# Kernel optimization log

Measured on AMD Instinct MI355X. Metric: run time of the kernel, lower is better.

Reference implementation:

```python
import jax, jax.numpy as jnp
import numpy as np

N_NODES = 100000
IN_DIM = 128
UNITS = 128
BATCH = 16384
N_NEIGH = 25


def setup_inputs() -> dict:
    key = jax.random.key(0)
    ks = jax.random.split(key, 6)
    features = jax.random.normal(ks[0], (N_NODES, IN_DIM), dtype=jnp.float32)
    node = jax.random.randint(ks[1], (BATCH, 1), 0, N_NODES)
    neighbours = jax.random.randint(ks[2], (BATCH, N_NEIGH), 0, N_NODES)
    # learned params
    def glorot(k, shape):
        lim = np.sqrt(6.0 / (shape[0] + shape[1]))
        return jax.random.uniform(k, shape, jnp.float32, -lim, lim)
    node_weights = glorot(ks[3], (IN_DIM, UNITS))
    lstm_W = glorot(ks[4], (IN_DIM, 4 * UNITS))   # kernel: gates [i, f, g, o]
    lstm_U = glorot(ks[5], (UNITS, 4 * UNITS))    # recurrent kernel
    lstm_b = jnp.ones((4 * UNITS,), jnp.float32)  # bias_initializer='ones'
    return {"features": features, "node": node, "neighbours": neighbours,
            "node_weights": node_weights, "lstm_W": lstm_W,
            "lstm_U": lstm_U, "lstm_b": lstm_b}


def _lstm_last_hidden(x_btd, W, U, b, units):
    # x_btd: [B, T, D] -> last hidden state [B, units]; Keras gate order i,f,g,o
    B = x_btd.shape[0]
    # precompute input projections for all steps: [T, B, 4U]
    zx = jnp.einsum('btd,dk->tbk', x_btd, W) + b

    def step(carry, zx_t):
        h, c = carry
        z = zx_t + h @ U
        i, f, g, o = jnp.split(z, 4, axis=-1)
        i = jax.nn.sigmoid(i)
        f = jax.nn.sigmoid(f)
        g = jnp.tanh(g)
        o = jax.nn.sigmoid(o)
        c = f * c + i * g
        h = o * jnp.tanh(c)
        return (h, c), None

    h0 = jnp.zeros((B, units), x_btd.dtype)
    c0 = jnp.zeros((B, units), x_btd.dtype)
    (h, _), _ = jax.lax.scan(step, (h0, c0), zx)
    return h


def reference(features, node, neighbours, node_weights, lstm_W, lstm_U, lstm_b):
    node_feat = features[node[:, 0]]          # [B, D]
    neigh_feat = features[neighbours]         # [B, T, D]
    from_neighs = _lstm_last_hidden(neigh_feat, lstm_W, lstm_U, lstm_b, UNITS)
    from_self = node_feat @ node_weights      # [B, units]
    output = (from_self + from_neighs) / 2
    return jax.nn.relu(output)
```

## Files before the change

kernel.cpp:

```cpp
#include <hip/hip_runtime.h>
#include <hip/hip_bf16.h>


typedef __bf16 bf16;
typedef __bf16 bf16x8 __attribute__((ext_vector_type(8)));
typedef float f32x4 __attribute__((ext_vector_type(4)));

#define FEATS_OFF 262144

__device__ __forceinline__ float fast_sig(float x) {
  float e = __builtin_amdgcn_exp2f(-1.442695041f * x);
  return __builtin_amdgcn_rcpf(1.0f + e);
}
__device__ __forceinline__ float fast_tanh(float x) {
  float e = __builtin_amdgcn_exp2f(-2.885390082f * x);
  return (1.0f - e) * __builtin_amdgcn_rcpf(1.0f + e);
}
__device__ __forceinline__ f32x4 splat4(float x) {
  f32x4 v; v[0] = x; v[1] = x; v[2] = x; v[3] = x; return v;
}
__device__ __forceinline__ bf16x8 pack8(float4 a, float4 b) {
  bf16x8 v;
  v[0] = (bf16)a.x; v[1] = (bf16)a.y; v[2] = (bf16)a.z; v[3] = (bf16)a.w;
  v[4] = (bf16)b.x; v[5] = (bf16)b.y; v[6] = (bf16)b.z; v[7] = (bf16)b.w;
  return v;
}

__global__ void prep_kernel(const float* __restrict__ W, const float* __restrict__ U,
                            const float* __restrict__ NW, bf16* __restrict__ ws) {
  int idx = blockIdx.x * 256 + threadIdx.x;
  if (idx < 131072) {
    const float* __restrict__ src = (idx < 65536) ? W : U;
    int r = idx & 65535;
    int f = r >> 9, lane = (r >> 3) & 63, j = r & 7;
    int kt = f & 3, g = (f >> 2) & 3, w = f >> 4;
    int k = kt * 32 + (lane >> 4) * 8 + j;
    int col = g * 128 + w * 16 + (lane & 15);
    ws[idx] = (bf16)src[k * 512 + col];
  } else {
    int r = idx - 131072;
    int f = r >> 9, lane = (r >> 3) & 63, j = r & 7;
    int kt = f & 3, w = f >> 2;
    int k = kt * 32 + (lane >> 4) * 8 + j;
    int col = w * 16 + (lane & 15);
    ws[idx] = (bf16)NW[k * 128 + col];
  }
}

__global__ void prep_feats(const float4* __restrict__ in, bf16x8* __restrict__ out) {
  int i = blockIdx.x * 256 + threadIdx.x;
  int stride = gridDim.x * 256;
  for (; i < 1600000; i += stride) {
    float4 a = in[2 * i], b = in[2 * i + 1];
    __builtin_nontemporal_store(pack8(a, b), out + i);
  }
}

__global__ __launch_bounds__(512, 2)
void lstm_kernel(const int* __restrict__ node, const int* __restrict__ neigh,
                 const float* __restrict__ bias, const bf16* __restrict__ wsf,
                 float* __restrict__ out) {
  __shared__ char ub[131072];
  __shared__ char xb[16384];
  __shared__ char hb[16384];

  const int tid  = threadIdx.x;
  const int lane = tid & 63;
  const int ug   = tid >> 6;
  const int l15  = lane & 15;
  const int lhi  = lane >> 4;
  const int b0   = blockIdx.x * 64;
  const bf16* __restrict__ fb = wsf + FEATS_OFF;

#pragma unroll
  for (int i = 0; i < 16; ++i) {
    int k = i * 512 + tid;
    ((bf16x8*)ub)[k] = *(const bf16x8*)(wsf + 65536 + k * 8);
  }

  float bb[4];
#pragma unroll
  for (int g = 0; g < 4; ++g) bb[g] = bias[g * 128 + ug * 16 + l15];

  f32x4 cc[4];
#pragma unroll
  for (int m = 0; m < 4; ++m) cc[m] = splat4(0.0f);

  const int gr = tid >> 3;
  const int gq = tid & 7;
  const int xsw = (gr & 7) << 4;
  const int xbase = gr * 256 + gq * 32;
  const int rbase = (b0 + gr) * 25;

  {
    int ni = neigh[rbase];
    const bf16* gsrc = fb + (size_t)ni * 128 + gq * 16;
    *(bf16x8*)(xb + (xbase ^ xsw))        = __builtin_nontemporal_load((const bf16x8*)gsrc);
    *(bf16x8*)(xb + ((xbase + 16) ^ xsw)) = __builtin_nontemporal_load((const bf16x8*)(gsrc + 8));
  }
  int ni_next = neigh[rbase + 1];
  __syncthreads();

  f32x4 acc[4][4];
  const int asw = (l15 & 7) << 4;

  auto mfma_phase = [&](const bf16x8 (&wf)[4][4], bool withH) {
#pragma unroll
    for (int kt = 0; kt < 4; ++kt) {
      bf16x8 ufr[4];
#pragma unroll
      for (int g = 0; g < 4; ++g)
        ufr[g] = *(const bf16x8*)(ub + (((ug * 16 + g * 4 + kt) << 6 | lane) << 4));
      bf16x8 xa[4];
#pragma unroll
      for (int m = 0; m < 4; ++m)
        xa[m] = *(const bf16x8*)(xb + (((m * 16 + l15) * 256 + (kt * 4 + lhi) * 16) ^ asw));
#pragma unroll
      for (int g = 0; g < 4; ++g)
#pragma unroll
        for (int m = 0; m < 4; ++m)
          acc[g][m] = __builtin_amdgcn_mfma_f32_16x16x32_bf16(xa[m], wf[g][kt], acc[g][m], 0, 0, 0);
      if (withH) {
        bf16x8 ha[4];
#pragma unroll
        for (int m = 0; m < 4; ++m)
          ha[m] = *(const bf16x8*)(hb + (((m * 16 + l15) * 256 + (kt * 4 + lhi) * 16) ^ asw));
#pragma unroll
        for (int g = 0; g < 4; ++g)
#pragma unroll
          for (int m = 0; m < 4; ++m)
            acc[g][m] = __builtin_amdgcn_mfma_f32_16x16x32_bf16(ha[m], ufr[g], acc[g][m], 0, 0, 0);
      }
    }
  };

#pragma unroll 1
  for (int t = 0; t < 24; ++t) {
    int ni = ni_next;
    ni_next = (t < 23) ? neigh[rbase + t + 2] : node[b0 + gr];

    bf16x8 wf[4][4];
#pragma unroll
    for (int g = 0; g < 4; ++g)
#pragma unroll
      for (int kt = 0; kt < 4; ++kt)
        wf[g][kt] = *(const bf16x8*)(wsf + (((ug * 4 + g) * 4 + kt) << 9) + (lane << 3));
    __builtin_amdgcn_sched_barrier(0);

    const bf16* gsrc = fb + (size_t)ni * 128 + gq * 16;
    bf16x8 pa = __builtin_nontemporal_load((const bf16x8*)gsrc);
    bf16x8 pb = __builtin_nontemporal_load((const bf16x8*)(gsrc + 8));

#pragma unroll
    for (int g = 0; g < 4; ++g) {
      f32x4 bi = splat4(bb[g]);
#pragma unroll
      for (int m = 0; m < 4; ++m) acc[g][m] = bi;
    }

    if (t == 0) mfma_phase(wf, false); else mfma_phase(wf, true);

    __syncthreads();

    *(bf16x8*)(xb + (xbase ^ xsw))        = pa;
    *(bf16x8*)(xb + ((xbase + 16) ^ xsw)) = pb;

#pragma unroll
    for (int m = 0; m < 4; ++m)
#pragma unroll
      for (int r = 0; r < 4; ++r) {
        float iv = fast_sig(acc[0][m][r]);
        float fv = fast_sig(acc[1][m][r]);
        float gv = fast_tanh(acc[2][m][r]);
        float ov = fast_sig(acc[3][m][r]);
        float cv = fv * cc[m][r] + iv * gv;
        cc[m][r] = cv;
        float hv = ov * fast_tanh(cv);
        int row = m * 16 + lhi * 4 + r;
        *(bf16*)(hb + ((row * 256 + (ug * 16 + l15) * 2) ^ ((row & 7) << 4))) = (bf16)hv;
      }
    __syncthreads();
  }

  float hl[4][4];
  {
    bf16x8 wf[4][4];
#pragma unroll
    for (int g = 0; g < 4; ++g)
#pragma unroll
      for (int kt = 0; kt < 4; ++kt)
        wf[g][kt] = *(const bf16x8*)(wsf + (((ug * 4 + g) * 4 + kt) << 9) + (lane << 3));
    __builtin_amdgcn_sched_barrier(0);

    const bf16* gsrc = fb + (size_t)ni_next * 128 + gq * 16;
    bf16x8 pa = __builtin_nontemporal_load((const bf16x8*)gsrc);
    bf16x8 pb = __builtin_nontemporal_load((const bf16x8*)(gsrc + 8));

#pragma unroll
    for (int g = 0; g < 4; ++g) {
      f32x4 bi = splat4(bb[g]);
#pragma unroll
      for (int m = 0; m < 4; ++m) acc[g][m] = bi;
    }
    mfma_phase(wf, true);

    __syncthreads();

    *(bf16x8*)(xb + (xbase ^ xsw))        = pa;
    *(bf16x8*)(xb + ((xbase + 16) ^ xsw)) = pb;

#pragma unroll
    for (int m = 0; m < 4; ++m)
#pragma unroll
      for (int r = 0; r < 4; ++r) {
        float iv = fast_sig(acc[0][m][r]);
        float fv = fast_sig(acc[1][m][r]);
        float gv = fast_tanh(acc[2][m][r]);
        float ov = fast_sig(acc[3][m][r]);
        float cv = fv * cc[m][r] + iv * gv;
        hl[m][r] = ov * fast_tanh(cv);
      }
    __syncthreads();
  }

  {
    f32x4 accs[4];
#pragma unroll
    for (int m = 0; m < 4; ++m) accs[m] = splat4(0.0f);
#pragma unroll
    for (int kt = 0; kt < 4; ++kt) {
      bf16x8 nwf = *(const bf16x8*)(wsf + 131072 + ((ug * 4 + kt) << 9) + (lane << 3));
      bf16x8 xa[4];
#pragma unroll
      for (int m = 0; m < 4; ++m)
        xa[m] = *(const bf16x8*)(xb + (((m * 16 + l15) * 256 + (kt * 4 + lhi) * 16) ^ asw));
#pragma unroll
      for (int m = 0; m < 4; ++m)
        accs[m] = __builtin_amdgcn_mfma_f32_16x16x32_bf16(xa[m], nwf, accs[m], 0, 0, 0);
    }
#pragma unroll
    for (int m = 0; m < 4; ++m)
#pragma unroll
      for (int r = 0; r < 4; ++r) {
        int row = m * 16 + lhi * 4 + r;
        float v = (accs[m][r] + hl[m][r]) * 0.5f;
        __builtin_nontemporal_store(v > 0.0f ? v : 0.0f,
                                    out + (b0 + row) * 128 + ug * 16 + l15);
      }
  }
}

extern "C" void kernel_launch(void* const* d_in, const int* in_sizes, int n_in,
                              void* d_out, int out_size, void* d_ws, size_t ws_size,
                              hipStream_t stream) {
  const float* feats = (const float*)d_in[0];
  const int*   node  = (const int*)d_in[1];
  const int*   neigh = (const int*)d_in[2];
  const float* nw    = (const float*)d_in[3];
  const float* W     = (const float*)d_in[4];
  const float* U     = (const float*)d_in[5];
  const float* b     = (const float*)d_in[6];
  bf16* ws = (bf16*)d_ws;
  float* out = (float*)d_out;

  prep_kernel<<<576, 256, 0, stream>>>(W, U, nw, ws);
  prep_feats<<<2048, 256, 0, stream>>>((const float4*)feats, (bf16x8*)(ws + FEATS_OFF));
  lstm_kernel<<<256, 512, 0, stream>>>(node, neigh, b, ws, out);
}
```

Measured before the change: 262.6 us.

## Gather neighbour features directly into registers and double-buffer hidden state

Each wave now loads its neighbour feature fragments straight from global memory into MFMA operand registers instead of staging them through shared memory. The hidden-state buffer is double-buffered so each timestep needs only one barrier. The two preprocessing kernels are merged into a single launch. The cost is that every wave redundantly fetches the whole x tile, raising cache traffic, and gather latency now sits inside each step.

```diff
diff --git a/kernel.cpp b/kernel.cpp
--- a/kernel.cpp
+++ b/kernel.cpp
@@ -26,33 +26,34 @@
   return v;
 }
 
-__global__ void prep_kernel(const float* __restrict__ W, const float* __restrict__ U,
-                            const float* __restrict__ NW, bf16* __restrict__ ws) {
-  int idx = blockIdx.x * 256 + threadIdx.x;
-  if (idx < 131072) {
-    const float* __restrict__ src = (idx < 65536) ? W : U;
-    int r = idx & 65535;
-    int f = r >> 9, lane = (r >> 3) & 63, j = r & 7;
-    int kt = f & 3, g = (f >> 2) & 3, w = f >> 4;
-    int k = kt * 32 + (lane >> 4) * 8 + j;
-    int col = g * 128 + w * 16 + (lane & 15);
-    ws[idx] = (bf16)src[k * 512 + col];
-  } else {
-    int r = idx - 131072;
-    int f = r >> 9, lane = (r >> 3) & 63, j = r & 7;
-    int kt = f & 3, w = f >> 2;
-    int k = kt * 32 + (lane >> 4) * 8 + j;
-    int col = w * 16 + (lane & 15);
-    ws[idx] = (bf16)NW[k * 128 + col];
-  }
-}
-
-__global__ void prep_feats(const float4* __restrict__ in, bf16x8* __restrict__ out) {
-  int i = blockIdx.x * 256 + threadIdx.x;
+__global__ void prep_all(const float* __restrict__ W, const float* __restrict__ U,
+                         const float* __restrict__ NW, const float4* __restrict__ feats,
+                         bf16* __restrict__ ws) {
+  int gid = blockIdx.x * 256 + threadIdx.x;
+  if (gid < 147456) {
+    int idx = gid;
+    if (idx < 131072) {
+      const float* __restrict__ src = (idx < 65536) ? W : U;
+      int r = idx & 65535;
+      int f = r >> 9, lane = (r >> 3) & 63, j = r & 7;
+      int kt = f & 3, g = (f >> 2) & 3, w = f >> 4;
+      int k = kt * 32 + (lane >> 4) * 8 + j;
+      int col = g * 128 + w * 16 + (lane & 15);
+      ws[idx] = (bf16)src[k * 512 + col];
+    } else {
+      int r = idx - 131072;
+      int f = r >> 9, lane = (r >> 3) & 63, j = r & 7;
+      int kt = f & 3, w = f >> 2;
+      int k = kt * 32 + (lane >> 4) * 8 + j;
+      int col = w * 16 + (lane & 15);
+      ws[idx] = (bf16)NW[k * 128 + col];
+    }
+  }
+  bf16x8* __restrict__ fo = (bf16x8*)(ws + FEATS_OFF);
   int stride = gridDim.x * 256;
-  for (; i < 1600000; i += stride) {
-    float4 a = in[2 * i], b = in[2 * i + 1];
-    __builtin_nontemporal_store(pack8(a, b), out + i);
+  for (int i = gid; i < 1600000; i += stride) {
+    float4 a = feats[2 * i], b = feats[2 * i + 1];
+    __builtin_nontemporal_store(pack8(a, b), fo + i);
   }
 }
 
@@ -61,8 +62,7 @@
                  const float* __restrict__ bias, const bf16* __restrict__ wsf,
                  float* __restrict__ out) {
   __shared__ char ub[131072];
-  __shared__ char xb[16384];
-  __shared__ char hb[16384];
+  __shared__ char hb[32768];
 
   const int tid  = threadIdx.x;
   const int lane = tid & 63;
@@ -86,45 +86,66 @@
 #pragma unroll
   for (int m = 0; m < 4; ++m) cc[m] = splat4(0.0f);
 
-  const int gr = tid >> 3;
-  const int gq = tid & 7;
-  const int xsw = (gr & 7) << 4;
-  const int xbase = gr * 256 + gq * 32;
-  const int rbase = (b0 + gr) * 25;
-
-  {
-    int ni = neigh[rbase];
-    const bf16* gsrc = fb + (size_t)ni * 128 + gq * 16;
-    *(bf16x8*)(xb + (xbase ^ xsw))        = __builtin_nontemporal_load((const bf16x8*)gsrc);
-    *(bf16x8*)(xb + ((xbase + 16) ^ xsw)) = __builtin_nontemporal_load((const bf16x8*)(gsrc + 8));
-  }
-  int ni_next = neigh[rbase + 1];
+  int niv[4];
+#pragma unroll
+  for (int m = 0; m < 4; ++m) niv[m] = neigh[(b0 + m * 16 + l15) * 25];
+
   __syncthreads();
 
   f32x4 acc[4][4];
   const int asw = (l15 & 7) << 4;
 
-  auto mfma_phase = [&](const bf16x8 (&wf)[4][4], bool withH) {
-#pragma unroll
-    for (int kt = 0; kt < 4; ++kt) {
-      bf16x8 ufr[4];
-#pragma unroll
-      for (int g = 0; g < 4; ++g)
-        ufr[g] = *(const bf16x8*)(ub + (((ug * 16 + g * 4 + kt) << 6 | lane) << 4));
-      bf16x8 xa[4];
-#pragma unroll
-      for (int m = 0; m < 4; ++m)
-        xa[m] = *(const bf16x8*)(xb + (((m * 16 + l15) * 256 + (kt * 4 + lhi) * 16) ^ asw));
-#pragma unroll
-      for (int g = 0; g < 4; ++g)
+  float hl[4][4];
+
+#pragma unroll 1
+  for (int t = 0; t < 25; ++t) {
+    const int pcur = t & 1;
+    const char* hrd = hb + pcur * 16384;
+    char*       hwr = hb + (pcur ^ 1) * 16384;
+
+    bf16x8 xa[4][4];
+#pragma unroll
+    for (int m = 0; m < 4; ++m) {
+      const bf16* bp = fb + (size_t)niv[m] * 128 + lhi * 8;
+#pragma unroll
+      for (int kt = 0; kt < 4; ++kt)
+        xa[m][kt] = __builtin_nontemporal_load((const bf16x8*)(bp + kt * 32));
+    }
+    bf16x8 wf[4][4];
+#pragma unroll
+    for (int g = 0; g < 4; ++g)
+#pragma unroll
+      for (int kt = 0; kt < 4; ++kt)
+        wf[g][kt] = *(const bf16x8*)(wsf + (((ug * 4 + g) * 4 + kt) << 9) + (lane << 3));
+    if (t < 24) {
+#pragma unroll
+      for (int m = 0; m < 4; ++m)
+        niv[m] = (t < 24 - 1) ? neigh[(b0 + m * 16 + l15) * 25 + t + 1]
+                              : neigh[(b0 + m * 16 + l15) * 25 + 24];
+    } else {
+#pragma unroll
+      for (int m = 0; m < 4; ++m) niv[m] = node[b0 + m * 16 + l15];
+    }
+    __builtin_amdgcn_sched_barrier(0);
+
+#pragma unroll
+    for (int g = 0; g < 4; ++g) {
+      f32x4 bi = splat4(bb[g]);
+#pragma unroll
+      for (int m = 0; m < 4; ++m) acc[g][m] = bi;
+    }
+
+    if (t > 0) {
+#pragma unroll
+      for (int kt = 0; kt < 4; ++kt) {
+        bf16x8 ufr[4];
+#pragma unroll
+        for (int g = 0; g < 4; ++g)
+          ufr[g] = *(const bf16x8*)(ub + (((ug * 16 + g * 4 + kt) << 6 | lane) << 4));
+        bf16x8 ha[4];
 #pragma unroll
         for (int m = 0; m < 4; ++m)
-          acc[g][m] = __builtin_amdgcn_mfma_f32_16x16x32_bf16(xa[m], wf[g][kt], acc[g][m], 0, 0, 0);
-      if (withH) {
-        bf16x8 ha[4];
-#pragma unroll
-        for (int m = 0; m < 4; ++m)
-          ha[m] = *(const bf16x8*)(hb + (((m * 16 + l15) * 256 + (kt * 4 + lhi) * 16) ^ asw));
+          ha[m] = *(const bf16x8*)(hrd + (((m * 16 + l15) * 256 + (kt * 4 + lhi) * 16) ^ asw));
 #pragma unroll
         for (int g = 0; g < 4; ++g)
 #pragma unroll
@@ -132,111 +153,64 @@
             acc[g][m] = __builtin_amdgcn_mfma_f32_16x16x32_bf16(ha[m], ufr[g], acc[g][m], 0, 0, 0);
       }
     }
-  };
-
-#pragma unroll 1
-  for (int t = 0; t < 24; ++t) {
-    int ni = ni_next;
-    ni_next = (t < 23) ? neigh[rbase + t + 2] : node[b0 + gr];
-
-    bf16x8 wf[4][4];
-#pragma unroll
-    for (int g = 0; g < 4; ++g)
+
+#pragma unroll
+    for (int kt = 0; kt < 4; ++kt)
+#pragma unroll
+      for (int g = 0; g < 4; ++g)
+#pragma unroll
+        for (int m = 0; m < 4; ++m)
+          acc[g][m] = __builtin_amdgcn_mfma_f32_16x16x32_bf16(xa[m][kt], wf[g][kt], acc[g][m], 0, 0, 0);
+
+    if (t < 24) {
+#pragma unroll
+      for (int m = 0; m < 4; ++m)
+#pragma unroll
+        for (int r = 0; r < 4; ++r) {
+          float iv = fast_sig(acc[0][m][r]);
+          float fv = fast_sig(acc[1][m][r]);
+          float gv = fast_tanh(acc[2][m][r]);
+          float ov = fast_sig(acc[3][m][r]);
+          float cv = fv * cc[m][r] + iv * gv;
+          cc[m][r] = cv;
+          float hv = ov * fast_tanh(cv);
+          int row = m * 16 + lhi * 4 + r;
+          *(bf16*)(hwr + ((row * 256 + (ug * 16 + l15) * 2) ^ ((row & 7) << 4))) = (bf16)hv;
+        }
+      __syncthreads();
+    } else {
+#pragma unroll
+      for (int m = 0; m < 4; ++m)
+#pragma unroll
+        for (int r = 0; r < 4; ++r) {
+          float iv = fast_sig(acc[0][m][r]);
+          float fv = fast_sig(acc[1][m][r]);
+          float gv = fast_tanh(acc[2][m][r]);
+          float ov = fast_sig(acc[3][m][r]);
+          float cv = fv * cc[m][r] + iv * gv;
+          hl[m][r] = ov * fast_tanh(cv);
+        }
+    }
+  }
+
+  {
+    bf16x8 xa[4][4];
+#pragma unroll
+    for (int m = 0; m < 4; ++m) {
+      const bf16* bp = fb + (size_t)niv[m] * 128 + lhi * 8;
 #pragma unroll
       for (int kt = 0; kt < 4; ++kt)
-        wf[g][kt] = *(const bf16x8*)(wsf + (((ug * 4 + g) * 4 + kt) << 9) + (lane << 3));
-    __builtin_amdgcn_sched_barrier(0);
-
-    const bf16* gsrc = fb + (size_t)ni * 128 + gq * 16;
-    bf16x8 pa = __builtin_nontemporal_load((const bf16x8*)gsrc);
-    bf16x8 pb = __builtin_nontemporal_load((const bf16x8*)(gsrc + 8));
-
-#pragma unroll
-    for (int g = 0; g < 4; ++g) {
-      f32x4 bi = splat4(bb[g]);
-#pragma unroll
-      for (int m = 0; m < 4; ++m) acc[g][m] = bi;
-    }
-
-    if (t == 0) mfma_phase(wf, false); else mfma_phase(wf, true);
-
-    __syncthreads();
-
-    *(bf16x8*)(xb + (xbase ^ xsw))        = pa;
-    *(bf16x8*)(xb + ((xbase + 16) ^ xsw)) = pb;
-
-#pragma unroll
-    for (int m = 0; m < 4; ++m)
-#pragma unroll
-      for (int r = 0; r < 4; ++r) {
-        float iv = fast_sig(acc[0][m][r]);
-        float fv = fast_sig(acc[1][m][r]);
-        float gv = fast_tanh(acc[2][m][r]);
-        float ov = fast_sig(acc[3][m][r]);
-        float cv = fv * cc[m][r] + iv * gv;
-        cc[m][r] = cv;
-        float hv = ov * fast_tanh(cv);
-        int row = m * 16 + lhi * 4 + r;
-        *(bf16*)(hb + ((row * 256 + (ug * 16 + l15) * 2) ^ ((row & 7) << 4))) = (bf16)hv;
-      }
-    __syncthreads();
-  }
-
-  float hl[4][4];
-  {
-    bf16x8 wf[4][4];
-#pragma unroll
-    for (int g = 0; g < 4; ++g)
-#pragma unroll
-      for (int kt = 0; kt < 4; ++kt)
-        wf[g][kt] = *(const bf16x8*)(wsf + (((ug * 4 + g) * 4 + kt) << 9) + (lane << 3));
-    __builtin_amdgcn_sched_barrier(0);
-
-    const bf16* gsrc = fb + (size_t)ni_next * 128 + gq * 16;
-    bf16x8 pa = __builtin_nontemporal_load((const bf16x8*)gsrc);
-    bf16x8 pb = __builtin_nontemporal_load((const bf16x8*)(gsrc + 8));
-
-#pragma unroll
-    for (int g = 0; g < 4; ++g) {
-      f32x4 bi = splat4(bb[g]);
-#pragma unroll
-      for (int m = 0; m < 4; ++m) acc[g][m] = bi;
-    }
-    mfma_phase(wf, true);
-
-    __syncthreads();
-
-    *(bf16x8*)(xb + (xbase ^ xsw))        = pa;
-    *(bf16x8*)(xb + ((xbase + 16) ^ xsw)) = pb;
-
-#pragma unroll
-    for (int m = 0; m < 4; ++m)
-#pragma unroll
-      for (int r = 0; r < 4; ++r) {
-        float iv = fast_sig(acc[0][m][r]);
-        float fv = fast_sig(acc[1][m][r]);
-        float gv = fast_tanh(acc[2][m][r]);
-        float ov = fast_sig(acc[3][m][r]);
-        float cv = fv * cc[m][r] + iv * gv;
-        hl[m][r] = ov * fast_tanh(cv);
-      }
-    __syncthreads();
-  }
-
-  {
+        xa[m][kt] = __builtin_nontemporal_load((const bf16x8*)(bp + kt * 32));
+    }
     f32x4 accs[4];
 #pragma unroll
     for (int m = 0; m < 4; ++m) accs[m] = splat4(0.0f);
 #pragma unroll
     for (int kt = 0; kt < 4; ++kt) {
       bf16x8 nwf = *(const bf16x8*)(wsf + 131072 + ((ug * 4 + kt) << 9) + (lane << 3));
-      bf16x8 xa[4];
-#pragma unroll
-      for (int m = 0; m < 4; ++m)
-        xa[m] = *(const bf16x8*)(xb + (((m * 16 + l15) * 256 + (kt * 4 + lhi) * 16) ^ asw));
-#pragma unroll
-      for (int m = 0; m < 4; ++m)
-        accs[m] = __builtin_amdgcn_mfma_f32_16x16x32_bf16(xa[m], nwf, accs[m], 0, 0, 0);
+#pragma unroll
+      for (int m = 0; m < 4; ++m)
+        accs[m] = __builtin_amdgcn_mfma_f32_16x16x32_bf16(xa[m][kt], nwf, accs[m], 0, 0, 0);
     }
 #pragma unroll
     for (int m = 0; m < 4; ++m)
@@ -263,7 +237,6 @@
   bf16* ws = (bf16*)d_ws;
   float* out = (float*)d_out;
 
-  prep_kernel<<<576, 256, 0, stream>>>(W, U, nw, ws);
-  prep_feats<<<2048, 256, 0, stream>>>((const float4*)feats, (bf16x8*)(ws + FEATS_OFF));
+  prep_all<<<2048, 256, 0, stream>>>(W, U, nw, (const float4*)feats, ws);
   lstm_kernel<<<256, 512, 0, stream>>>(node, neigh, b, ws, out);
 }
```

New measurement: 407.9 us. 55.4% more time.

## Drop feature bf16 precast; gather fp32 rows directly and double-buffer LDS

Applied to the files above, without the earlier changes.

Removes the prep_feats pass that converted the whole 100k x 128 feature table to bf16, and instead gathers the needed fp32 rows inside the LSTM kernel, converting them in registers. The recurrent weights U move from a 128KB LDS staging buffer into per-thread registers, and the x/h LDS buffers become double-buffered so one barrier per step suffices instead of two. This avoids reading and writing the full feature table when only about 426k rows are used. In exchange, each gather moves twice the bytes, and holding U in registers raises register pressure under the 512x2 launch bounds, which could cause spills.

```diff
diff --git a/kernel.cpp b/kernel.cpp
--- a/kernel.cpp
+++ b/kernel.cpp
@@ -6,8 +6,6 @@
 typedef __bf16 bf16x8 __attribute__((ext_vector_type(8)));
 typedef float f32x4 __attribute__((ext_vector_type(4)));
 
-#define FEATS_OFF 262144
-
 __device__ __forceinline__ float fast_sig(float x) {
   float e = __builtin_amdgcn_exp2f(-1.442695041f * x);
   return __builtin_amdgcn_rcpf(1.0f + e);
@@ -19,15 +17,15 @@
 __device__ __forceinline__ f32x4 splat4(float x) {
   f32x4 v; v[0] = x; v[1] = x; v[2] = x; v[3] = x; return v;
 }
-__device__ __forceinline__ bf16x8 pack8(float4 a, float4 b) {
+__device__ __forceinline__ bf16x8 pack8(f32x4 a, f32x4 b) {
   bf16x8 v;
-  v[0] = (bf16)a.x; v[1] = (bf16)a.y; v[2] = (bf16)a.z; v[3] = (bf16)a.w;
-  v[4] = (bf16)b.x; v[5] = (bf16)b.y; v[6] = (bf16)b.z; v[7] = (bf16)b.w;
+  v[0] = (bf16)a[0]; v[1] = (bf16)a[1]; v[2] = (bf16)a[2]; v[3] = (bf16)a[3];
+  v[4] = (bf16)b[0]; v[5] = (bf16)b[1]; v[6] = (bf16)b[2]; v[7] = (bf16)b[3];
   return v;
 }
 
-__global__ void prep_kernel(const float* __restrict__ W, const float* __restrict__ U,
-                            const float* __restrict__ NW, bf16* __restrict__ ws) {
+__global__ void prep_weights(const float* __restrict__ W, const float* __restrict__ U,
+                             const float* __restrict__ NW, bf16* __restrict__ ws) {
   int idx = blockIdx.x * 256 + threadIdx.x;
   if (idx < 131072) {
     const float* __restrict__ src = (idx < 65536) ? W : U;
@@ -47,22 +45,12 @@
   }
 }
 
-__global__ void prep_feats(const float4* __restrict__ in, bf16x8* __restrict__ out) {
-  int i = blockIdx.x * 256 + threadIdx.x;
-  int stride = gridDim.x * 256;
-  for (; i < 1600000; i += stride) {
-    float4 a = in[2 * i], b = in[2 * i + 1];
-    __builtin_nontemporal_store(pack8(a, b), out + i);
-  }
-}
-
 __global__ __launch_bounds__(512, 2)
-void lstm_kernel(const int* __restrict__ node, const int* __restrict__ neigh,
-                 const float* __restrict__ bias, const bf16* __restrict__ wsf,
-                 float* __restrict__ out) {
-  __shared__ char ub[131072];
-  __shared__ char xb[16384];
-  __shared__ char hb[16384];
+void lstm_kernel(const float* __restrict__ feats, const int* __restrict__ node,
+                 const int* __restrict__ neigh, const float* __restrict__ bias,
+                 const bf16* __restrict__ wsf, float* __restrict__ out) {
+  __shared__ char xb[2][16384];
+  __shared__ char hb[2][16384];
 
   const int tid  = threadIdx.x;
   const int lane = tid & 63;
@@ -70,13 +58,13 @@
   const int l15  = lane & 15;
   const int lhi  = lane >> 4;
   const int b0   = blockIdx.x * 64;
-  const bf16* __restrict__ fb = wsf + FEATS_OFF;
-
-#pragma unroll
-  for (int i = 0; i < 16; ++i) {
-    int k = i * 512 + tid;
-    ((bf16x8*)ub)[k] = *(const bf16x8*)(wsf + 65536 + k * 8);
-  }
+
+  bf16x8 uf[4][4];
+#pragma unroll
+  for (int g = 0; g < 4; ++g)
+#pragma unroll
+    for (int kt = 0; kt < 4; ++kt)
+      uf[g][kt] = *(const bf16x8*)(wsf + 65536 + (((ug * 4 + g) * 4 + kt) << 9) + (lane << 3));
 
   float bb[4];
 #pragma unroll
@@ -94,9 +82,13 @@
 
   {
     int ni = neigh[rbase];
-    const bf16* gsrc = fb + (size_t)ni * 128 + gq * 16;
-    *(bf16x8*)(xb + (xbase ^ xsw))        = __builtin_nontemporal_load((const bf16x8*)gsrc);
-    *(bf16x8*)(xb + ((xbase + 16) ^ xsw)) = __builtin_nontemporal_load((const bf16x8*)(gsrc + 8));
+    const f32x4* gs = (const f32x4*)(feats + (size_t)ni * 128 + gq * 16);
+    f32x4 f0 = __builtin_nontemporal_load(gs + 0);
+    f32x4 f1 = __builtin_nontemporal_load(gs + 1);
+    f32x4 f2 = __builtin_nontemporal_load(gs + 2);
+    f32x4 f3 = __builtin_nontemporal_load(gs + 3);
+    *(bf16x8*)(xb[0] + (xbase ^ xsw))        = pack8(f0, f1);
+    *(bf16x8*)(xb[0] + ((xbase + 16) ^ xsw)) = pack8(f2, f3);
   }
   int ni_next = neigh[rbase + 1];
   __syncthreads();
@@ -104,66 +96,65 @@
   f32x4 acc[4][4];
   const int asw = (l15 & 7) << 4;
 
-  auto mfma_phase = [&](const bf16x8 (&wf)[4][4], bool withH) {
+#pragma unroll 1
+  for (int t = 0; t < 24; ++t) {
+    const int p = t & 1;
+    const char* xrd = xb[p];
+    const char* hrd = hb[p];
+    char*       xwr = xb[p ^ 1];
+    char*       hwr = hb[p ^ 1];
+
+    int ni = ni_next;
+    ni_next = (t < 23) ? neigh[rbase + t + 2] : node[b0 + gr];
+
+    bf16x8 wf[4][4];
+#pragma unroll
+    for (int g = 0; g < 4; ++g)
+#pragma unroll
+      for (int kt = 0; kt < 4; ++kt)
+        wf[g][kt] = *(const bf16x8*)(wsf + (((ug * 4 + g) * 4 + kt) << 9) + (lane << 3));
+    __builtin_amdgcn_sched_barrier(0);
+
+    const f32x4* gs = (const f32x4*)(feats + (size_t)ni * 128 + gq * 16);
+    f32x4 f0 = __builtin_nontemporal_load(gs + 0);
+    f32x4 f1 = __builtin_nontemporal_load(gs + 1);
+    f32x4 f2 = __builtin_nontemporal_load(gs + 2);
+    f32x4 f3 = __builtin_nontemporal_load(gs + 3);
+    __builtin_amdgcn_sched_barrier(0);
+
+#pragma unroll
+    for (int g = 0; g < 4; ++g) {
+      f32x4 bi = splat4(bb[g]);
+#pragma unroll
+      for (int m = 0; m < 4; ++m) acc[g][m] = bi;
+    }
+
 #pragma unroll
     for (int kt = 0; kt < 4; ++kt) {
-      bf16x8 ufr[4];
-#pragma unroll
-      for (int g = 0; g < 4; ++g)
-        ufr[g] = *(const bf16x8*)(ub + (((ug * 16 + g * 4 + kt) << 6 | lane) << 4));
       bf16x8 xa[4];
 #pragma unroll
       for (int m = 0; m < 4; ++m)
-        xa[m] = *(const bf16x8*)(xb + (((m * 16 + l15) * 256 + (kt * 4 + lhi) * 16) ^ asw));
+        xa[m] = *(const bf16x8*)(xrd + (((m * 16 + l15) * 256 + (kt * 4 + lhi) * 16) ^ asw));
 #pragma unroll
       for (int g = 0; g < 4; ++g)
 #pragma unroll
         for (int m = 0; m < 4; ++m)
           acc[g][m] = __builtin_amdgcn_mfma_f32_16x16x32_bf16(xa[m], wf[g][kt], acc[g][m], 0, 0, 0);
-      if (withH) {
+      if (t > 0) {
         bf16x8 ha[4];
 #pragma unroll
         for (int m = 0; m < 4; ++m)
-          ha[m] = *(const bf16x8*)(hb + (((m * 16 + l15) * 256 + (kt * 4 + lhi) * 16) ^ asw));
+          ha[m] = *(const bf16x8*)(hrd + (((m * 16 + l15) * 256 + (kt * 4 + lhi) * 16) ^ asw));
 #pragma unroll
         for (int g = 0; g < 4; ++g)
 #pragma unroll
           for (int m = 0; m < 4; ++m)
-            acc[g][m] = __builtin_amdgcn_mfma_f32_16x16x32_bf16(ha[m], ufr[g], acc[g][m], 0, 0, 0);
-      }
-    }
-  };
-
-#pragma unroll 1
-  for (int t = 0; t < 24; ++t) {
-    int ni = ni_next;
-    ni_next = (t < 23) ? neigh[rbase + t + 2] : node[b0 + gr];
-
-    bf16x8 wf[4][4];
-#pragma unroll
-    for (int g = 0; g < 4; ++g)
-#pragma unroll
-      for (int kt = 0; kt < 4; ++kt)
-        wf[g][kt] = *(const bf16x8*)(wsf + (((ug * 4 + g) * 4 + kt) << 9) + (lane << 3));
-    __builtin_amdgcn_sched_barrier(0);
-
-    const bf16* gsrc = fb + (size_t)ni * 128 + gq * 16;
-    bf16x8 pa = __builtin_nontemporal_load((const bf16x8*)gsrc);
-    bf16x8 pb = __builtin_nontemporal_load((const bf16x8*)(gsrc + 8));
-
-#pragma unroll
-    for (int g = 0; g < 4; ++g) {
-      f32x4 bi = splat4(bb[g]);
-#pragma unroll
-      for (int m = 0; m < 4; ++m) acc[g][m] = bi;
-    }
-
-    if (t == 0) mfma_phase(wf, false); else mfma_phase(wf, true);
-
-    __syncthreads();
-
-    *(bf16x8*)(xb + (xbase ^ xsw))        = pa;
-    *(bf16x8*)(xb + ((xbase + 16) ^ xsw)) = pb;
+            acc[g][m] = __builtin_amdgcn_mfma_f32_16x16x32_bf16(ha[m], uf[g][kt], acc[g][m], 0, 0, 0);
+      }
+    }
+
+    *(bf16x8*)(xwr + (xbase ^ xsw))        = pack8(f0, f1);
+    *(bf16x8*)(xwr + ((xbase + 16) ^ xsw)) = pack8(f2, f3);
 
 #pragma unroll
     for (int m = 0; m < 4; ++m)
@@ -177,13 +168,17 @@
         cc[m][r] = cv;
         float hv = ov * fast_tanh(cv);
         int row = m * 16 + lhi * 4 + r;
-        *(bf16*)(hb + ((row * 256 + (ug * 16 + l15) * 2) ^ ((row & 7) << 4))) = (bf16)hv;
-      }
+        *(bf16*)(hwr + ((row * 256 + (ug * 16 + l15) * 2) ^ ((row & 7) << 4))) = (bf16)hv;
+      }
+
     __syncthreads();
   }
 
   float hl[4][4];
   {
+    const char* xrd = xb[0];
+    const char* hrd = hb[0];
+
     bf16x8 wf[4][4];
 #pragma unroll
     for (int g = 0; g < 4; ++g)
@@ -192,9 +187,12 @@
         wf[g][kt] = *(const bf16x8*)(wsf + (((ug * 4 + g) * 4 + kt) << 9) + (lane << 3));
     __builtin_amdgcn_sched_barrier(0);
 
-    const bf16* gsrc = fb + (size_t)ni_next * 128 + gq * 16;
-    bf16x8 pa = __builtin_nontemporal_load((const bf16x8*)gsrc);
-    bf16x8 pb = __builtin_nontemporal_load((const bf16x8*)(gsrc + 8));
+    const f32x4* gs = (const f32x4*)(feats + (size_t)ni_next * 128 + gq * 16);
+    f32x4 f0 = __builtin_nontemporal_load(gs + 0);
+    f32x4 f1 = __builtin_nontemporal_load(gs + 1);
+    f32x4 f2 = __builtin_nontemporal_load(gs + 2);
+    f32x4 f3 = __builtin_nontemporal_load(gs + 3);
+    __builtin_amdgcn_sched_barrier(0);
 
 #pragma unroll
     for (int g = 0; g < 4; ++g) {
@@ -202,12 +200,25 @@
 #pragma unroll
       for (int m = 0; m < 4; ++m) acc[g][m] = bi;
     }
-    mfma_phase(wf, true);
-
-    __syncthreads();
-
-    *(bf16x8*)(xb + (xbase ^ xsw))        = pa;
-    *(bf16x8*)(xb + ((xbase + 16) ^ xsw)) = pb;
+#pragma unroll
+    for (int kt = 0; kt < 4; ++kt) {
+      bf16x8 xa[4], ha[4];
+#pragma unroll
+      for (int m = 0; m < 4; ++m) {
+        xa[m] = *(const bf16x8*)(xrd + (((m * 16 + l15) * 256 + (kt * 4 + lhi) * 16) ^ asw));
+        ha[m] = *(const bf16x8*)(hrd + (((m * 16 + l15) * 256 + (kt * 4 + lhi) * 16) ^ asw));
+      }
+#pragma unroll
+      for (int g = 0; g < 4; ++g)
+#pragma unroll
+        for (int m = 0; m < 4; ++m) {
+          acc[g][m] = __builtin_amdgcn_mfma_f32_16x16x32_bf16(xa[m], wf[g][kt], acc[g][m], 0, 0, 0);
+          acc[g][m] = __builtin_amdgcn_mfma_f32_16x16x32_bf16(ha[m], uf[g][kt], acc[g][m], 0, 0, 0);
+        }
+    }
+
+    *(bf16x8*)(xb[1] + (xbase ^ xsw))        = pack8(f0, f1);
+    *(bf16x8*)(xb[1] + ((xbase + 16) ^ xsw)) = pack8(f2, f3);
 
 #pragma unroll
     for (int m = 0; m < 4; ++m)
@@ -233,7 +244,7 @@
       bf16x8 xa[4];
 #pragma unroll
       for (int m = 0; m < 4; ++m)
-        xa[m] = *(const bf16x8*)(xb + (((m * 16 + l15) * 256 + (kt * 4 + lhi) * 16) ^ asw));
+        xa[m] = *(const bf16x8*)(xb[1] + (((m * 16 + l15) * 256 + (kt * 4 + lhi) * 16) ^ asw));
 #pragma unroll
       for (int m = 0; m < 4; ++m)
         accs[m] = __builtin_amdgcn_mfma_f32_16x16x32_bf16(xa[m], nwf, accs[m], 0, 0, 0);
@@ -263,7 +274,6 @@
   bf16* ws = (bf16*)d_ws;
   float* out = (float*)d_out;
 
-  prep_kernel<<<576, 256, 0, stream>>>(W, U, nw, ws);
-  prep_feats<<<2048, 256, 0, stream>>>((const float4*)feats, (bf16x8*)(ws + FEATS_OFF));
-  lstm_kernel<<<256, 512, 0, stream>>>(node, neigh, b, ws, out);
-}
+  prep_weights<<<576, 256, 0, stream>>>(W, U, nw, ws);
+  lstm_kernel<<<256, 512, 0, stream>>>(feats, node, neigh, b, ws, out);
+}
```

New measurement: 409.6 us. 1.56x slower.
